# Performance work log

Measured on AMD Instinct MI355X. Metric: run time of the kernel, lower is better.

Reference implementation:

```python
import jax, jax.numpy as jnp
import numpy as np

B, L, HID = 2, 2048, 1024
H = 16
D = HID // H          # head_dim = 64
LR = 16               # gate low-rank dim
EPS = 1e-5
GLN = 16.0            # gate_logit_normalizer
SCALE = D ** -0.5


def setup_inputs() -> dict:
    key = jax.random.key(0)
    ks = jax.random.split(key, 9)
    s = 0.02
    return {
        "x": jax.random.normal(ks[0], (B, L, HID), jnp.float32),
        "Wq": jax.random.normal(ks[1], (HID, HID), jnp.float32) * s,
        "Wk": jax.random.normal(ks[2], (HID, HID), jnp.float32) * s,
        "Wv": jax.random.normal(ks[3], (HID, HID), jnp.float32) * s,
        "Wg1": jax.random.normal(ks[4], (HID, LR), jnp.float32) * s,
        "Wg2": jax.random.normal(ks[5], (LR, HID), jnp.float32) * s,
        "bg2": jnp.zeros((HID,), jnp.float32),
        "Wg": jax.random.normal(ks[6], (HID, HID), jnp.float32) * s,
        "g_norm_w": jnp.ones((D,), jnp.float32),
        "Wo": jax.random.normal(ks[7], (HID, HID), jnp.float32) * s,
    }


def reference(x, Wq, Wk, Wv, Wg1, Wg2, bg2, Wg, g_norm_w, Wo):
    Bb, Ll, Hid = x.shape
    q = (x @ Wq).reshape(Bb, Ll, H, D)
    k = (x @ Wk).reshape(Bb, Ll, H, D)
    v = (x @ Wv).reshape(Bb, Ll, H, D)
    gk = jax.nn.log_sigmoid(((x @ Wg1) @ Wg2 + bg2)).reshape(Bb, Ll, H, D) / GLN

    def step(S, inp):
        q_t, k_t, v_t, gk_t = inp  # each (B, H, D)
        # S: (B,H,D,D); gate broadcasts over the v-dim (last axis)
        S = jnp.exp(gk_t)[..., None] * S + k_t[..., None] * v_t[..., None, :]
        o_t = jnp.einsum('bhdv,bhd->bhv', S, q_t) * SCALE  # S^T @ q / sqrt(D)
        return S, o_t

    S0 = jnp.zeros((Bb, H, D, D), x.dtype)
    scan_in = tuple(jnp.moveaxis(t, 1, 0) for t in (q, k, v, gk))  # (L,B,H,D)
    S, o = jax.lax.scan(step, S0, scan_in)
    o = jnp.moveaxis(o, 0, 1)  # (B, L, H, D)

    # RMSNorm over head_dim with affine weight
    o = o * jax.lax.rsqrt(jnp.mean(o * o, axis=-1, keepdims=True) + EPS) * g_norm_w
    o = o.reshape(Bb, Ll, Hid)

    # Swish output gate
    g = x @ Wg
    o = o * (g * jax.nn.sigmoid(g))
    o = o @ Wo
    return o, S[:, None]  # last_state: (B,1,H,D,D)
```

## Files before the change

### kernel.cpp

```cpp
#include <hip/hip_runtime.h>
#include <hip/hip_bf16.h>

typedef unsigned short u16;
typedef __attribute__((ext_vector_type(8))) short bf16x8;
typedef __attribute__((ext_vector_type(4))) float f32x4;

#define L_SEQ 2048
#define HID 1024
#define NC 32
#define MTOK 4096
#define GEPS 1e-5f
#define QSCALE 0.125f

__device__ __forceinline__ float bf2f(u16 u){ union{unsigned i; float f;}c; c.i=(unsigned)u<<16; return c.f; }
__device__ __forceinline__ u16 f2bf(float f){ union{__hip_bfloat16 h; u16 u;}c; c.h=__float2bfloat16(f); return c.u; }

__device__ __forceinline__ int swz72(int row, int col){ return row * 72 + (col ^ ((row >> 1) & 24)); }
__device__ __forceinline__ int swzc(int t){ return ((t >> 2) & 3) << 3; }

__device__ __forceinline__ void gload_lds16(const u16* g, u16* l){
  __builtin_amdgcn_global_load_lds((const __attribute__((address_space(1))) void*)g,
                                   (__attribute__((address_space(3))) void*)l, 16, 0, 0);
}

__global__ __launch_bounds__(256) void gla_prep(const float* __restrict__ x,
                                                u16* __restrict__ xb,
                                                const float* W0, const float* W1,
                                                const float* W2, const float* W3,
                                                const float* W4,
                                                u16* D0, u16* D1, u16* D2, u16* D3, u16* D4){
  __shared__ float tile[32][33];
  int bid = blockIdx.x;
  if (bid < 2048){
    size_t i = ((size_t)bid * 256 + threadIdx.x) * 8;
    float4 a = *(const float4*)&x[i];
    float4 b = *(const float4*)&x[i + 4];
    u16 o[8] __attribute__((aligned(16))) = {
      f2bf(a.x), f2bf(a.y), f2bf(a.z), f2bf(a.w),
      f2bf(b.x), f2bf(b.y), f2bf(b.z), f2bf(b.w) };
    *(uint4*)&xb[i] = *(uint4*)o;
  } else {
    int id = bid - 2048;
    int z = id >> 10, rem = id & 1023;
    int bx = rem & 31, by = rem >> 5;
    const float* W; u16* D;
    switch (z){
      case 0: W = W0; D = D0; break;
      case 1: W = W1; D = D1; break;
      case 2: W = W2; D = D2; break;
      case 3: W = W3; D = D3; break;
      default: W = W4; D = D4; break;
    }
    int tx = threadIdx.x & 31, ty = threadIdx.x >> 5;
    int n0 = bx * 32, k0 = by * 32;
    #pragma unroll
    for (int r = ty; r < 32; r += 8)
      tile[r][tx] = W[(size_t)(k0 + r) * HID + n0 + tx];
    __syncthreads();
    #pragma unroll
    for (int r = ty; r < 32; r += 8)
      D[(size_t)(n0 + r) * HID + k0 + tx] = f2bf(tile[tx][r]);
  }
}

__global__ __launch_bounds__(256) void gla_xg1_mfma(const u16* __restrict__ xb,
                                                    const float* __restrict__ Wg1,
                                                    float* __restrict__ xg1){
  __shared__ u16 WL[16 * 1032];
  #pragma unroll 8
  for (int i = 0; i < 64; i++){
    int flat = i * 256 + threadIdx.x;
    int k = flat >> 4, n = flat & 15;
    WL[n * 1032 + k] = f2bf(Wg1[flat]);
  }
  __syncthreads();
  int lane = threadIdx.x & 63, w = threadIdx.x >> 6;
  int lr = lane & 15, lk = lane >> 4;
  int rt = blockIdx.x * 4 + w;
  const u16* Arow = xb + ((size_t)rt * 16 + lr) * HID;
  f32x4 acc;
  #pragma unroll
  for (int e = 0; e < 4; e++) acc[e] = 0.f;
  #pragma unroll 4
  for (int ks = 0; ks < 32; ks++){
    bf16x8 a = *(const bf16x8*)&Arow[ks * 32 + lk * 8];
    bf16x8 b = *(const bf16x8*)&WL[lr * 1032 + ks * 32 + lk * 8];
    acc = __builtin_amdgcn_mfma_f32_16x16x32_bf16(a, b, acc, 0, 0, 0);
  }
  #pragma unroll
  for (int r = 0; r < 4; r++)
    xg1[(size_t)(rt * 16 + lk * 4 + r) * 16 + lr] = acc[r];
}

__global__ __launch_bounds__(256) void gla_gkcg2(const float* __restrict__ xg1,
                                                 const float* __restrict__ Wg2,
                                                 const float* __restrict__ bg2,
                                                 u16* __restrict__ CG){
  __shared__ float xs[64][17];
  __shared__ float wg[16][64];
  __shared__ float lss[64][65];
  __shared__ float red[4][64];
  int blk = blockIdx.x;
  int bc = blk >> 4, cgi = blk & 15;
  int b = bc >> 5, c = bc & 31;
  int col0 = cgi * 64;
  int tok0 = b * L_SEQ + c * 64;
  int tid = threadIdx.x;
  {
    int row = tid >> 2, e4 = (tid & 3) * 4;
    float4 v = *(const float4*)&xg1[(size_t)(tok0 + row) * 16 + e4];
    xs[row][e4 + 0] = v.x; xs[row][e4 + 1] = v.y;
    xs[row][e4 + 2] = v.z; xs[row][e4 + 3] = v.w;
    int f = tid * 4; int r = f >> 6, cc = f & 63;
    *(float4*)&wg[r][cc] = *(const float4*)&Wg2[(size_t)r * HID + col0 + cc];
  }
  __syncthreads();
  int t = tid & 63, cq = tid >> 6;
  float xr[16];
  #pragma unroll
  for (int r = 0; r < 16; r++) xr[r] = xs[t][r];
  #pragma unroll
  for (int i = 0; i < 16; i++){
    int col = cq * 16 + i;
    float z = bg2[col0 + col];
    #pragma unroll
    for (int r = 0; r < 16; r++) z += xr[r] * wg[r][col];
    lss[t][col] = -__logf(1.f + __expf(-z)) * (1.0f / 16.0f);
  }
  __syncthreads();
  int col = tid & 63, q = tid >> 6;
  float cum16[16];
  float s = 0.f;
  #pragma unroll
  for (int i = 0; i < 16; i++){ s += lss[q * 16 + i][col]; cum16[i] = s; }
  red[q][col] = s;
  __syncthreads();
  float offs = 0.f;
  #pragma unroll
  for (int p = 0; p < 3; p++) if (p < q) offs += red[p][col];
  #pragma unroll
  for (int i = 0; i < 16; i++)
    CG[(size_t)(tok0 + q * 16 + i) * HID + col0 + col] = f2bf(offs + cum16[i]);
}

__global__ __launch_bounds__(512) void gla_gemm_qkvg(const u16* __restrict__ A,
                                                     const u16* __restrict__ Bt,
                                                     u16* __restrict__ C){
  constexpr int NT = HID / 32;
  __shared__ u16 As[2][256 * 32];
  __shared__ u16 Bs[2][128 * 32];
  const int tid = threadIdx.x;
  const int lane = tid & 63, wid = tid >> 6;
  const int wm = wid >> 1, wn = wid & 1;
  const int lr = lane & 15, lk = lane >> 4;
  const int id = blockIdx.x + 16 * blockIdx.y;
  const int nid = (id & 7) * 64 + (id >> 3);
  const int bm = nid & 15, bn = nid >> 4;
  const int srow = tid >> 2;
  const int skw  = ((tid & 3) * 8) ^ ((srow & 3) << 3);
  const u16* Ag = A  + ((size_t)bm * 256 + srow) * HID + skw;
  const u16* Bg = Bt + ((size_t)bn * 128 + srow) * HID + skw;

  f32x4 acc[4][4];
  #pragma unroll
  for (int i = 0; i < 4; i++)
    #pragma unroll
    for (int j = 0; j < 4; j++)
      #pragma unroll
      for (int e = 0; e < 4; e++) acc[i][j][e] = 0.f;

  auto STAGE = [&](int buf, int kt){
    gload_lds16(Ag + kt * 32,                         &As[buf][tid * 8]);
    gload_lds16(Ag + (size_t)128 * HID + kt * 32,     &As[buf][4096 + tid * 8]);
    gload_lds16(Bg + kt * 32,                         &Bs[buf][tid * 8]);
  };

  STAGE(0, 0);
  for (int t = 0; t < NT; ++t){
    const int buf = t & 1;
    if (t + 1 < NT){
      STAGE(buf ^ 1, t + 1);
      asm volatile("s_waitcnt vmcnt(3)\ns_barrier" ::: "memory");
    } else {
      asm volatile("s_waitcnt vmcnt(0)\ns_barrier" ::: "memory");
    }
    bf16x8 af[4], bfr[4];
    #pragma unroll
    for (int m = 0; m < 4; m++){
      int row = wm * 64 + m * 16 + lr;
      af[m] = *(const bf16x8*)&As[buf][(row * 32 + lk * 8) ^ ((row & 3) << 3)];
    }
    #pragma unroll
    for (int n = 0; n < 4; n++){
      int row = wn * 64 + n * 16 + lr;
      bfr[n] = *(const bf16x8*)&Bs[buf][(row * 32 + lk * 8) ^ ((row & 3) << 3)];
    }
    __builtin_amdgcn_s_setprio(1);
    #pragma unroll
    for (int m = 0; m < 4; m++)
      #pragma unroll
      for (int n = 0; n < 4; n++)
        acc[m][n] = __builtin_amdgcn_mfma_f32_16x16x32_bf16(af[m], bfr[n], acc[m][n], 0, 0, 0);
    __builtin_amdgcn_s_setprio(0);
    __builtin_amdgcn_sched_barrier(0);
    asm volatile("s_barrier" ::: "memory");
  }

  #pragma unroll
  for (int i = 0; i < 4; i++)
    #pragma unroll
    for (int j = 0; j < 4; j++){
      int row0 = bm * 256 + wm * 64 + i * 16 + lk * 4;
      int cb   = bn * 128 + wn * 64 + j * 16 + lr;
      int sel  = cb >> 10, col = cb & 1023;
      size_t base = (size_t)sel * ((size_t)MTOK * HID) + (size_t)row0 * HID + col;
      #pragma unroll
      for (int r = 0; r < 4; r++)
        C[base + (size_t)r * HID] = f2bf(acc[i][j][r]);
    }
}

__global__ __launch_bounds__(256) void gla_gemm_out2(const u16* __restrict__ A,
                                                     const u16* __restrict__ Bt,
                                                     float* __restrict__ C){
  constexpr int NT = 16;
  __shared__ __align__(16) char smem[49152];
  const int tid = threadIdx.x;
  const int lane = tid & 63, wid = tid >> 6;
  const int kg = wid >> 1, w = wid & 1;
  const int lr = lane & 15, lk = lane >> 4;
  const int bm = blockIdx.x, bn = blockIdx.y;
  const int srow = tid >> 2;
  const int skw  = ((tid & 3) * 8) ^ ((srow & 3) << 3);
  const u16* Ag = A  + ((size_t)bm * 64  + srow) * HID + skw;
  const u16* Bg = Bt + ((size_t)bn * 128 + srow) * HID + skw;
  auto seg = [&](int g, int buf) -> u16* { return (u16*)(smem + (g * 2 + buf) * 12288); };

  f32x4 acc[4][4];
  #pragma unroll
  for (int i = 0; i < 4; i++)
    #pragma unroll
    for (int j = 0; j < 4; j++)
      #pragma unroll
      for (int e = 0; e < 4; e++) acc[i][j][e] = 0.f;

  auto STAGE = [&](int buf, int kt){
    gload_lds16(Ag + kt * 32,                          seg(0, buf) + tid * 8);
    gload_lds16(Bg + kt * 32,                          seg(0, buf) + 2048 + tid * 8);
    gload_lds16(Bg + (size_t)64 * HID + kt * 32,       seg(0, buf) + 4096 + tid * 8);
    gload_lds16(Ag + 512 + kt * 32,                    seg(1, buf) + tid * 8);
    gload_lds16(Bg + 512 + kt * 32,                    seg(1, buf) + 2048 + tid * 8);
    gload_lds16(Bg + (size_t)64 * HID + 512 + kt * 32, seg(1, buf) + 4096 + tid * 8);
  };

  STAGE(0, 0);
  for (int t = 0; t < NT; ++t){
    const int buf = t & 1;
    if (t + 1 < NT){
      STAGE(buf ^ 1, t + 1);
      asm volatile("s_waitcnt vmcnt(6)\ns_barrier" ::: "memory");
    } else {
      asm volatile("s_waitcnt vmcnt(0)\ns_barrier" ::: "memory");
    }
    const u16* Ab = seg(kg, buf);
    const u16* Bb = seg(kg, buf) + 2048;
    bf16x8 af[4], bfr[4];
    #pragma unroll
    for (int m = 0; m < 4; m++){
      int row = m * 16 + lr;
      af[m] = *(const bf16x8*)&Ab[(row * 32 + lk * 8) ^ ((row & 3) << 3)];
    }
    #pragma unroll
    for (int n = 0; n < 4; n++){
      int row = w * 64 + n * 16 + lr;
      bfr[n] = *(const bf16x8*)&Bb[(row * 32 + lk * 8) ^ ((row & 3) << 3)];
    }
    __builtin_amdgcn_s_setprio(1);
    #pragma unroll
    for (int m = 0; m < 4; m++)
      #pragma unroll
      for (int n = 0; n < 4; n++)
        acc[m][n] = __builtin_amdgcn_mfma_f32_16x16x32_bf16(af[m], bfr[n], acc[m][n], 0, 0, 0);
    __builtin_amdgcn_s_setprio(0);
    __builtin_amdgcn_sched_barrier(0);
    asm volatile("s_barrier" ::: "memory");
  }

  float* red = (float*)smem;
  if (kg == 1){
    #pragma unroll
    for (int m = 0; m < 4; m++)
      #pragma unroll
      for (int n = 0; n < 4; n++){
        int lrow = m * 16 + lk * 4, lcol = w * 64 + n * 16 + lr;
        #pragma unroll
        for (int r = 0; r < 4; r++)
          red[(lrow + r) * 132 + lcol] = acc[m][n][r];
      }
  }
  __syncthreads();
  if (kg == 0){
    #pragma unroll
    for (int m = 0; m < 4; m++)
      #pragma unroll
      for (int n = 0; n < 4; n++){
        int lrow = m * 16 + lk * 4, lcol = w * 64 + n * 16 + lr;
        #pragma unroll
        for (int r = 0; r < 4; r++)
          C[(size_t)(bm * 64 + lrow + r) * HID + bn * 128 + lcol] =
              acc[m][n][r] + red[(lrow + r) * 132 + lcol];
      }
  }
}

__global__ __launch_bounds__(256) void gla_chunk_state2(const u16* __restrict__ Kb,
                                                        const u16* __restrict__ Vb,
                                                        const u16* __restrict__ CG,
                                                        u16* __restrict__ Tbuf,
                                                        float* __restrict__ Dbuf){
  __shared__ u16 KHT[64 * 72];
  __shared__ u16 VT[64 * 72];
  int blk = blockIdx.x;
  int c = blk & (NC - 1), bh = blk >> 5;
  int b = bh >> 4, h = bh & 15;
  int tid = threadIdx.x;
  int lane = tid & 63, w = tid >> 6;
  int lr = lane & 15, lk = lane >> 4;
  int tr = tid >> 2, tc = (tid & 3) * 16;
  size_t gbase = ((size_t)(b * L_SEQ + c * 64)) * HID + h * 64;

  float cg[16], cgl[16];
  {
    const u16* cgp = CG + gbase + (size_t)tr * HID + tc;
    const u16* clp = CG + gbase + (size_t)63 * HID + tc;
    uint4 a0 = *(const uint4*)cgp, a1 = *(const uint4*)(cgp + 8);
    uint4 l0 = *(const uint4*)clp, l1 = *(const uint4*)(clp + 8);
    const u16* au = (const u16*)&a0; const u16* au2 = (const u16*)&a1;
    const u16* lu = (const u16*)&l0; const u16* lu2 = (const u16*)&l1;
    #pragma unroll
    for (int e = 0; e < 8; e++){
      cg[e] = bf2f(au[e]); cg[8 + e] = bf2f(au2[e]);
      cgl[e] = bf2f(lu[e]); cgl[8 + e] = bf2f(lu2[e]);
    }
  }
  {
    const u16* kp = Kb + gbase + (size_t)tr * HID + tc;
    const u16* vp = Vb + gbase + (size_t)tr * HID + tc;
    uint4 kr0 = *(const uint4*)kp, kr1 = *(const uint4*)(kp + 8);
    uint4 vr0 = *(const uint4*)vp, vr1 = *(const uint4*)(vp + 8);
    const u16* ku = (const u16*)&kr0; const u16* ku2 = (const u16*)&kr1;
    const u16* vu = (const u16*)&vr0; const u16* vu2 = (const u16*)&vr1;
    #pragma unroll
    for (int e = 0; e < 8; e++){
      KHT[swz72(tc + e, tr)]     = f2bf(bf2f(ku[e])  * __expf(cgl[e]     - cg[e]));
      KHT[swz72(tc + 8 + e, tr)] = f2bf(bf2f(ku2[e]) * __expf(cgl[8 + e] - cg[8 + e]));
      VT[swz72(tc + e, tr)]      = vu[e];
      VT[swz72(tc + 8 + e, tr)]  = vu2[e];
    }
  }
  if (tr == 0){
    #pragma unroll
    for (int e = 0; e < 16; e++)
      Dbuf[(size_t)blk * 64 + tc + e] = __expf(cgl[e]);
  }
  __syncthreads();
  int R0 = w * 16;
  f32x4 tacc[4];
  #pragma unroll
  for (int v = 0; v < 4; v++)
    #pragma unroll
    for (int e = 0; e < 4; e++) tacc[v][e] = 0.f;
  #pragma unroll
  for (int ks = 0; ks < 2; ks++){
    bf16x8 a = *(const bf16x8*)&KHT[swz72(R0 + lr, ks * 32 + lk * 8)];
    #pragma unroll
    for (int v0 = 0; v0 < 4; v0++){
      bf16x8 bb = *(const bf16x8*)&VT[swz72(v0 * 16 + lr, ks * 32 + lk * 8)];
      tacc[v0] = __builtin_amdgcn_mfma_f32_16x16x32_bf16(a, bb, tacc[v0], 0, 0, 0);
    }
  }
  u16* Tp = Tbuf + (size_t)blk * 4096;
  #pragma unroll
  for (int v0 = 0; v0 < 4; v0++){
    int d = R0 + lk * 4, v = v0 * 16 + lr;
    #pragma unroll
    for (int r = 0; r < 4; r++)
      Tp[(d + r) * 64 + v] = f2bf(tacc[v0][r]);
  }
}

__global__ __launch_bounds__(256) void gla_state_scan2(const u16* __restrict__ Tbuf,
                                                       const float* __restrict__ Dbuf,
                                                       float* __restrict__ Sfin,
                                                       u16* __restrict__ Sinb){
  int bh = blockIdx.x >> 4, seg = blockIdx.x & 15;
  int dv = seg * 256 + threadIdx.x;
  int d = dv >> 6;
  float S = 0.f;
  for (int c = 0; c < NC; c++){
    size_t slot = (size_t)bh * NC + c;
    float t  = bf2f(Tbuf[slot * 4096 + dv]);
    float dec = Dbuf[slot * 64 + d];
    Sinb[slot * 4096 + dv] = f2bf(S);
    S = dec * S + t;
  }
  Sfin[(size_t)bh * 4096 + dv] = S;
}

__global__ __launch_bounds__(256) void gla_chunk_out2(const u16* __restrict__ Qb,
                                                      const u16* __restrict__ Kb,
                                                      const u16* __restrict__ Vb,
                                                      const u16* __restrict__ CG,
                                                      const u16* __restrict__ Sinb,
                                                      const u16* __restrict__ Gb,
                                                      const float* __restrict__ gnw,
                                                      u16* __restrict__ OG){
  __shared__ u16 QT[64 * 72];
  __shared__ u16 KP[64 * 72];
  __shared__ u16 VT[64 * 72];
  __shared__ u16 ST[64 * 72];
  int blk = blockIdx.x;
  int c = blk & (NC - 1), bh = blk >> 5;
  int b = bh >> 4, h = bh & 15;
  int tid = threadIdx.x;
  int lane = tid & 63, w = tid >> 6;
  int lr = lane & 15, lk = lane >> 4;
  int tr = tid >> 2, tc = (tid & 3) * 16;
  int R0 = w * 16;
  size_t gbase = ((size_t)(b * L_SEQ + c * 64)) * HID + h * 64;

  u16 gpre[16];
  {
    float cg[16];
    const u16* cgp = CG + gbase + (size_t)tr * HID + tc;
    uint4 a0 = *(const uint4*)cgp, a1 = *(const uint4*)(cgp + 8);
    const u16* au = (const u16*)&a0; const u16* au2 = (const u16*)&a1;
    #pragma unroll
    for (int e = 0; e < 8; e++){ cg[e] = bf2f(au[e]); cg[8 + e] = bf2f(au2[e]); }
    const u16* qp = Qb + gbase + (size_t)tr * HID + tc;
    const u16* kp = Kb + gbase + (size_t)tr * HID + tc;
    const u16* vp = Vb + gbase + (size_t)tr * HID + tc;
    uint4 qr0 = *(const uint4*)qp, qr1 = *(const uint4*)(qp + 8);
    uint4 kr0 = *(const uint4*)kp, kr1 = *(const uint4*)(kp + 8);
    uint4 vr0 = *(const uint4*)vp, vr1 = *(const uint4*)(vp + 8);
    #pragma unroll
    for (int r = 0; r < 4; r++)
      #pragma unroll
      for (int v0 = 0; v0 < 4; v0++)
        gpre[r * 4 + v0] = Gb[gbase + (size_t)(R0 + lk * 4 + r) * HID + v0 * 16 + lr];
    const u16* qu = (const u16*)&qr0; const u16* qu2 = (const u16*)&qr1;
    const u16* ku = (const u16*)&kr0; const u16* ku2 = (const u16*)&kr1;
    const u16* vu = (const u16*)&vr0; const u16* vu2 = (const u16*)&vr1;
    u16 qt[16] __attribute__((aligned(16)));
    u16 kt[16] __attribute__((aligned(16)));
    #pragma unroll
    for (int e = 0; e < 8; e++){
      float ec0 = __expf(cg[e]),  ei0 = __expf(-cg[e]);
      float ec1 = __expf(cg[8+e]), ei1 = __expf(-cg[8+e]);
      qt[e]     = f2bf(bf2f(qu[e])  * ec0 * QSCALE);
      qt[8 + e] = f2bf(bf2f(qu2[e]) * ec1 * QSCALE);
      kt[e]     = f2bf(bf2f(ku[e])  * ei0);
      kt[8 + e] = f2bf(bf2f(ku2[e]) * ei1);
      VT[swz72(tc + e, tr)]     = vu[e];
      VT[swz72(tc + 8 + e, tr)] = vu2[e];
    }
    *(uint4*)&QT[tr * 72 + tc]     = *(uint4*)&qt[0];
    *(uint4*)&QT[tr * 72 + tc + 8] = *(uint4*)&qt[8];
    *(uint4*)&KP[tr * 72 + tc]     = *(uint4*)&kt[0];
    *(uint4*)&KP[tr * 72 + tc + 8] = *(uint4*)&kt[8];
    const u16* sp = Sinb + (size_t)blk * 4096 + (size_t)tr * 64 + tc;
    uint4 s0 = *(const uint4*)sp, s1 = *(const uint4*)(sp + 8);
    const u16* su = (const u16*)&s0; const u16* su2 = (const u16*)&s1;
    #pragma unroll
    for (int e = 0; e < 8; e++){
      ST[swz72(tc + e, tr)]     = su[e];
      ST[swz72(tc + 8 + e, tr)] = su2[e];
    }
  }
  __syncthreads();

  f32x4 pacc[4];
  #pragma unroll
  for (int j = 0; j < 4; j++)
    #pragma unroll
    for (int e = 0; e < 4; e++) pacc[j][e] = 0.f;
  #pragma unroll
  for (int ks = 0; ks < 2; ks++){
    bf16x8 a = *(const bf16x8*)&QT[(R0 + lr) * 72 + ks * 32 + lk * 8];
    #pragma unroll
    for (int j0 = 0; j0 < 4; j0++){
      bf16x8 bb = *(const bf16x8*)&KP[(j0 * 16 + lr) * 72 + ks * 32 + lk * 8];
      pacc[j0] = __builtin_amdgcn_mfma_f32_16x16x32_bf16(a, bb, pacc[j0], 0, 0, 0);
    }
  }
  __syncthreads();

  #pragma unroll
  for (int j0 = 0; j0 < 4; j0++){
    int j = j0 * 16 + lr;
    #pragma unroll
    for (int r = 0; r < 4; r++){
      int t = R0 + lk * 4 + r;
      KP[t * 72 + (j ^ swzc(t))] = (j <= t) ? f2bf(pacc[j0][r]) : (u16)0;
    }
  }

  f32x4 oacc[4];
  #pragma unroll
  for (int v = 0; v < 4; v++)
    #pragma unroll
    for (int e = 0; e < 4; e++) oacc[v][e] = 0.f;
  #pragma unroll
  for (int ks = 0; ks < 2; ks++){
    bf16x8 a = *(const bf16x8*)&QT[(R0 + lr) * 72 + ks * 32 + lk * 8];
    #pragma unroll
    for (int v0 = 0; v0 < 4; v0++){
      bf16x8 bb = *(const bf16x8*)&ST[swz72(v0 * 16 + lr, ks * 32 + lk * 8)];
      oacc[v0] = __builtin_amdgcn_mfma_f32_16x16x32_bf16(a, bb, oacc[v0], 0, 0, 0);
    }
  }
  #pragma unroll
  for (int ks = 0; ks < 2; ks++){
    int arow = R0 + lr;
    bf16x8 a = *(const bf16x8*)&KP[arow * 72 + ((ks * 32 + lk * 8) ^ swzc(arow))];
    #pragma unroll
    for (int v0 = 0; v0 < 4; v0++){
      bf16x8 bb = *(const bf16x8*)&VT[swz72(v0 * 16 + lr, ks * 32 + lk * 8)];
      oacc[v0] = __builtin_amdgcn_mfma_f32_16x16x32_bf16(a, bb, oacc[v0], 0, 0, 0);
    }
  }

  {
    float gnv[4];
    #pragma unroll
    for (int v0 = 0; v0 < 4; v0++) gnv[v0] = gnw[v0 * 16 + lr];
    #pragma unroll
    for (int r = 0; r < 4; r++){
      float ssq = 0.f;
      #pragma unroll
      for (int v0 = 0; v0 < 4; v0++) ssq += oacc[v0][r] * oacc[v0][r];
      ssq += __shfl_xor(ssq, 1, 64);
      ssq += __shfl_xor(ssq, 2, 64);
      ssq += __shfl_xor(ssq, 4, 64);
      ssq += __shfl_xor(ssq, 8, 64);
      float rn = rsqrtf(ssq * (1.0f / 64.0f) + GEPS);
      int t = R0 + lk * 4 + r;
      u16* orow = OG + gbase + (size_t)t * HID;
      #pragma unroll
      for (int v0 = 0; v0 < 4; v0++){
        float g = bf2f(gpre[r * 4 + v0]);
        float sw = g / (1.f + __expf(-g));
        orow[v0 * 16 + lr] = f2bf(oacc[v0][r] * rn * gnv[v0] * sw);
      }
    }
  }
}

extern "C" void kernel_launch(void* const* d_in, const int* in_sizes, int n_in,
                              void* d_out, int out_size, void* d_ws, size_t ws_size,
                              hipStream_t stream){
  (void)in_sizes; (void)n_in; (void)out_size;
  const float* x   = (const float*)d_in[0];
  const float* Wq  = (const float*)d_in[1];
  const float* Wk  = (const float*)d_in[2];
  const float* Wv  = (const float*)d_in[3];
  const float* Wg1 = (const float*)d_in[4];
  const float* Wg2 = (const float*)d_in[5];
  const float* bg2 = (const float*)d_in[6];
  const float* Wg  = (const float*)d_in[7];
  const float* gnw = (const float*)d_in[8];
  const float* Wo  = (const float*)d_in[9];
  float* out = (float*)d_out;

  char* ws = (char*)d_ws;
  size_t off = 0;
  auto alloc = [&](size_t bytes) -> char* {
    char* p = ws + off; off += (bytes + 255) & ~(size_t)255; return p;
  };
  u16* xb   = (u16*)alloc((size_t)MTOK * HID * 2);
  u16* WTq  = (u16*)alloc((size_t)HID * HID * 2);
  u16* WTk  = (u16*)alloc((size_t)HID * HID * 2);
  u16* WTv  = (u16*)alloc((size_t)HID * HID * 2);
  u16* WTg  = (u16*)alloc((size_t)HID * HID * 2);
  u16* WTo  = (u16*)alloc((size_t)HID * HID * 2);
  u16* Qb   = (u16*)alloc((size_t)MTOK * HID * 2);
  u16* Kb   = (u16*)alloc((size_t)MTOK * HID * 2);
  u16* Vb   = (u16*)alloc((size_t)MTOK * HID * 2);
  u16* Gb   = (u16*)alloc((size_t)MTOK * HID * 2);
  u16* CGb  = (u16*)alloc((size_t)MTOK * HID * 2);
  float* xg1b = (float*)alloc((size_t)MTOK * 16 * 4);
  u16* Tbuf = (u16*)alloc((size_t)1024 * 4096 * 2);
  float* Dbuf = (float*)alloc((size_t)1024 * 64 * 4);
  u16* Sinb = (u16*)alloc((size_t)1024 * 4096 * 2);
  u16* OG   = (u16*)alloc((size_t)MTOK * HID * 2);
  if (off > ws_size) return;

  gla_prep<<<7168, 256, 0, stream>>>(x, xb, Wq, Wk, Wv, Wg, Wo,
                                     WTq, WTk, WTv, WTg, WTo);
  gla_xg1_mfma<<<64, 256, 0, stream>>>(xb, Wg1, xg1b);
  gla_gkcg2<<<1024, 256, 0, stream>>>(xg1b, Wg2, bg2, CGb);

  dim3 gq(16, 32);
  gla_gemm_qkvg<<<gq, 512, 0, stream>>>(xb, WTq, Qb);

  gla_chunk_state2<<<1024, 256, 0, stream>>>(Kb, Vb, CGb, Tbuf, Dbuf);
  gla_state_scan2<<<512, 256, 0, stream>>>(Tbuf, Dbuf, out + (size_t)MTOK * HID, Sinb);
  gla_chunk_out2<<<1024, 256, 0, stream>>>(Qb, Kb, Vb, CGb, Sinb, Gb, gnw, OG);

  dim3 go(64, 8);
  gla_gemm_out2<<<go, 256, 0, stream>>>(OG, WTo, out);
}
```

Measured before the change: 116.3 us.

## Fold x@Wg1 into prep kernel and triple-buffer the QKVG GEMM loads

The low-rank gate projection x@Wg1 moves into the prep kernel. It reads fp32 x directly and converts it to bf16 in registers, which removes one kernel launch and its dependency on xb. The QKVG GEMM mainloop goes from double to triple buffering in LDS, prefetching two k-tiles ahead to hide global load latency. The cost is more LDS per block, which may reduce occupancy, and uncached, uncoalesced strided reads of Wg1 in the 64 gate blocks.

```diff
diff --git a/kernel.cpp b/kernel.cpp
--- a/kernel.cpp
+++ b/kernel.cpp
@@ -25,14 +25,39 @@
 
 __global__ __launch_bounds__(256) void gla_prep(const float* __restrict__ x,
                                                 u16* __restrict__ xb,
+                                                const float* __restrict__ Wg1,
+                                                float* __restrict__ xg1,
                                                 const float* W0, const float* W1,
                                                 const float* W2, const float* W3,
                                                 const float* W4,
                                                 u16* D0, u16* D1, u16* D2, u16* D3, u16* D4){
   __shared__ float tile[32][33];
   int bid = blockIdx.x;
-  if (bid < 2048){
-    size_t i = ((size_t)bid * 256 + threadIdx.x) * 8;
+  if (bid < 64){
+    int lane = threadIdx.x & 63, w = threadIdx.x >> 6;
+    int lr = lane & 15, lk = lane >> 4;
+    int rt = bid * 4 + w;
+    const float* Arow = x + ((size_t)rt * 16 + lr) * HID;
+    f32x4 acc;
+    #pragma unroll
+    for (int e = 0; e < 4; e++) acc[e] = 0.f;
+    for (int ks = 0; ks < 32; ks++){
+      float4 a0 = *(const float4*)&Arow[ks * 32 + lk * 8];
+      float4 a1 = *(const float4*)&Arow[ks * 32 + lk * 8 + 4];
+      u16 av[8] __attribute__((aligned(16))) = {
+        f2bf(a0.x), f2bf(a0.y), f2bf(a0.z), f2bf(a0.w),
+        f2bf(a1.x), f2bf(a1.y), f2bf(a1.z), f2bf(a1.w) };
+      u16 bv[8] __attribute__((aligned(16)));
+      #pragma unroll
+      for (int e = 0; e < 8; e++)
+        bv[e] = f2bf(Wg1[(size_t)(ks * 32 + lk * 8 + e) * 16 + lr]);
+      acc = __builtin_amdgcn_mfma_f32_16x16x32_bf16(*(bf16x8*)av, *(bf16x8*)bv, acc, 0, 0, 0);
+    }
+    #pragma unroll
+    for (int r = 0; r < 4; r++)
+      xg1[(size_t)(rt * 16 + lk * 4 + r) * 16 + lr] = acc[r];
+  } else if (bid < 2112){
+    size_t i = ((size_t)(bid - 64) * 256 + threadIdx.x) * 8;
     float4 a = *(const float4*)&x[i];
     float4 b = *(const float4*)&x[i + 4];
     u16 o[8] __attribute__((aligned(16))) = {
@@ -40,7 +65,7 @@
       f2bf(b.x), f2bf(b.y), f2bf(b.z), f2bf(b.w) };
     *(uint4*)&xb[i] = *(uint4*)o;
   } else {
-    int id = bid - 2048;
+    int id = bid - 2112;
     int z = id >> 10, rem = id & 1023;
     int bx = rem & 31, by = rem >> 5;
     const float* W; u16* D;
@@ -61,35 +86,6 @@
     for (int r = ty; r < 32; r += 8)
       D[(size_t)(n0 + r) * HID + k0 + tx] = f2bf(tile[tx][r]);
   }
-}
-
-__global__ __launch_bounds__(256) void gla_xg1_mfma(const u16* __restrict__ xb,
-                                                    const float* __restrict__ Wg1,
-                                                    float* __restrict__ xg1){
-  __shared__ u16 WL[16 * 1032];
-  #pragma unroll 8
-  for (int i = 0; i < 64; i++){
-    int flat = i * 256 + threadIdx.x;
-    int k = flat >> 4, n = flat & 15;
-    WL[n * 1032 + k] = f2bf(Wg1[flat]);
-  }
-  __syncthreads();
-  int lane = threadIdx.x & 63, w = threadIdx.x >> 6;
-  int lr = lane & 15, lk = lane >> 4;
-  int rt = blockIdx.x * 4 + w;
-  const u16* Arow = xb + ((size_t)rt * 16 + lr) * HID;
-  f32x4 acc;
-  #pragma unroll
-  for (int e = 0; e < 4; e++) acc[e] = 0.f;
-  #pragma unroll 4
-  for (int ks = 0; ks < 32; ks++){
-    bf16x8 a = *(const bf16x8*)&Arow[ks * 32 + lk * 8];
-    bf16x8 b = *(const bf16x8*)&WL[lr * 1032 + ks * 32 + lk * 8];
-    acc = __builtin_amdgcn_mfma_f32_16x16x32_bf16(a, b, acc, 0, 0, 0);
-  }
-  #pragma unroll
-  for (int r = 0; r < 4; r++)
-    xg1[(size_t)(rt * 16 + lk * 4 + r) * 16 + lr] = acc[r];
 }
 
 __global__ __launch_bounds__(256) void gla_gkcg2(const float* __restrict__ xg1,
@@ -147,8 +143,8 @@
                                                      const u16* __restrict__ Bt,
                                                      u16* __restrict__ C){
   constexpr int NT = HID / 32;
-  __shared__ u16 As[2][256 * 32];
-  __shared__ u16 Bs[2][128 * 32];
+  __shared__ u16 As[3][256 * 32];
+  __shared__ u16 Bs[3][128 * 32];
   const int tid = threadIdx.x;
   const int lane = tid & 63, wid = tid >> 6;
   const int wm = wid >> 1, wn = wid & 1;
@@ -176,10 +172,13 @@
   };
 
   STAGE(0, 0);
+  STAGE(1, 1);
   for (int t = 0; t < NT; ++t){
-    const int buf = t & 1;
-    if (t + 1 < NT){
-      STAGE(buf ^ 1, t + 1);
+    const int buf = t % 3;
+    if (t + 2 < NT){
+      STAGE((t + 2) % 3, t + 2);
+      asm volatile("s_waitcnt vmcnt(6)\ns_barrier" ::: "memory");
+    } else if (t + 1 < NT){
       asm volatile("s_waitcnt vmcnt(3)\ns_barrier" ::: "memory");
     } else {
       asm volatile("s_waitcnt vmcnt(0)\ns_barrier" ::: "memory");
@@ -595,9 +594,8 @@
   u16* OG   = (u16*)alloc((size_t)MTOK * HID * 2);
   if (off > ws_size) return;
 
-  gla_prep<<<7168, 256, 0, stream>>>(x, xb, Wq, Wk, Wv, Wg, Wo,
+  gla_prep<<<7232, 256, 0, stream>>>(x, xb, Wg1, xg1b, Wq, Wk, Wv, Wg, Wo,
                                      WTq, WTk, WTv, WTg, WTo);
-  gla_xg1_mfma<<<64, 256, 0, stream>>>(xb, Wg1, xg1b);
   gla_gkcg2<<<1024, 256, 0, stream>>>(xg1b, Wg2, bg2, CGb);
 
   dim3 gq(16, 32);
```

Result: no change. 115.7 us (-0.5%).
